# Kernel optimization log

Hardware: AMD Instinct MI355X
Metric: run time of the kernel (lower is better)

## Reference

```python
import jax, jax.numpy as jnp
import numpy as np

LMAX = 6
F_IN = 512      # sphere_fdim
F_HID = 8       # f_hidden
N_PTS = 192     # s2 healpix grid points (projector & feature-sphere kernel)
N_SO3GRID = 4000  # SO3Activation grid (resolution=10, ~20x10x20)
N_CONVGRID = 192  # so3_near_identity_grid (8 alpha x 3 beta x 8 gamma)
S2_DIM = (LMAX + 1) ** 2                            # 49
SO3_DIM = sum((2 * l + 1) ** 2 for l in range(LMAX + 1))  # 455
B = 128
C_ENC = 2048
H = W = 7


def setup_inputs() -> dict:
    key = jax.random.key(0)
    ks = jax.random.split(key, 11)
    return {
        "fmap": jax.random.normal(ks[0], (B, C_ENC, H, W), jnp.float32),
        "conv_w": jax.random.normal(ks[1], (F_IN, C_ENC), jnp.float32) / np.sqrt(C_ENC).astype(np.float32),
        "conv_b": jnp.zeros((F_IN,), jnp.float32),
        "proj_w": jax.random.uniform(ks[2], (H, W, N_PTS), jnp.float32) / (H * W),
        "proj_Y": jax.random.normal(ks[3], (N_PTS, S2_DIM), jnp.float32),
        "fs_w": jax.random.normal(ks[4], (F_IN, F_HID, N_PTS), jnp.float32),
        "fs_Y": jax.random.normal(ks[5], (N_PTS, S2_DIM), jnp.float32),
        "act_to": jax.random.normal(ks[6], (SO3_DIM, N_SO3GRID), jnp.float32) / np.sqrt(SO3_DIM).astype(np.float32),
        "act_from": jax.random.normal(ks[7], (N_SO3GRID, SO3_DIM), jnp.float32) / np.float32(N_SO3GRID),
        "so3_w": jax.random.normal(ks[8], (F_HID, 1, N_CONVGRID), jnp.float32),
        "so3_D": jax.random.normal(ks[9], (N_CONVGRID, SO3_DIM), jnp.float32),
    }


def _s2_to_so3_linear(x, psi, f_in):
    # e3nn o3.Linear(s2_irreps -> so3_irreps, internal_weights=False).
    # x: (B, f_in, S2_DIM) with per-l blocks of size 2l+1 (mul=1).
    # psi: (f_in, f_out, S2_DIM). Per l: outer product of input irrep with
    # weight irrep -> (2l+1)x(2l+1) Wigner block; path norm 1/sqrt(f_in*mul_in).
    outs = []
    for l in range(LMAX + 1):
        s, e = l * l, (l + 1) ** 2
        xl = x[:, :, s:e]          # (B, f_in, 2l+1)
        wl = psi[:, :, s:e]        # (f_in, f_out, 2l+1)
        ol = jnp.einsum('bfm,fgu->bgum', xl, wl) / np.sqrt(f_in).astype(np.float32)
        outs.append(ol.reshape(ol.shape[0], ol.shape[1], -1))
    return jnp.concatenate(outs, axis=-1)   # (B, f_out, SO3_DIM)


def _so3_to_so3_linear(x, psi, f_in):
    # e3nn o3.Linear(so3_irreps -> so3_irreps, internal_weights=False).
    # x: (B, f_in, SO3_DIM), per-l block (mul=2l+1, dim=2l+1) flattened [u, m].
    # psi: (f_in, f_out, SO3_DIM), per-l block (u_in, u_out).
    outs = []
    off = 0
    for l in range(LMAX + 1):
        d = 2 * l + 1
        xl = x[:, :, off:off + d * d].reshape(x.shape[0], f_in, d, d)
        wl = psi[:, :, off:off + d * d].reshape(f_in, psi.shape[1], d, d)
        ol = jnp.einsum('bfum,fguv->bgvm', xl, wl) / np.sqrt(f_in * d).astype(np.float32)
        outs.append(ol.reshape(ol.shape[0], ol.shape[1], -1))
        off += d * d
    return jnp.concatenate(outs, axis=-1)


def reference(fmap, conv_w, conv_b, proj_w, proj_Y, fs_w, fs_Y, act_to, act_from, so3_w, so3_D):
    # --- SpatialS2Projector: 1x1 conv, orthographic-grid weighting, S2 FT ---
    x = jnp.einsum('bchw,fc->bfhw', fmap, conv_w) + conv_b[None, :, None, None]
    x = jnp.einsum('bfhw,hwn->bfn', x, proj_w)                   # (B, 512, N_PTS)
    x = jnp.einsum('bfn,ni->bfi', x, proj_Y) / np.sqrt(N_PTS).astype(np.float32)  # (B, 512, 49)
    # --- feature sphere -> external weight for o3.Linear (S2 conv theorem) ---
    psi = jnp.einsum('fgn,ni->fgi', fs_w, fs_Y) / np.sqrt(N_PTS).astype(np.float32)  # (512, 8, 49)
    x = _s2_to_so3_linear(x, psi, F_IN)                          # (B, 8, 455)
    # --- SO3Activation: synthesize signal on SO3 grid, relu, analyze back ---
    g = jax.nn.relu(jnp.einsum('bfi,in->bfn', x, act_to))        # (B, 8, N_SO3GRID)
    x = jnp.einsum('bfn,ni->bfi', g, act_from)                   # (B, 8, 455)
    # --- SO3Convolution over near-identity grid ---
    psi2 = jnp.einsum('fgn,ni->fgi', so3_w, so3_D) / np.sqrt(N_CONVGRID).astype(np.float32)  # (8, 1, 455)
    x = _so3_to_so3_linear(x, psi2, F_HID)                       # (B, 1, 455)
    return x
```

## Files before the change

kernel.cpp:

```cpp
#include <hip/hip_runtime.h>
#include <hip/hip_bf16.h>

#define NB    128
#define CENC  2048
#define FIN   512
#define FHID  8
#define S2D   49
#define SO3D  455
#define HW    49

typedef unsigned short ushort_t;
typedef __bf16 bf16x8 __attribute__((ext_vector_type(8)));
typedef float  f32x4  __attribute__((ext_vector_type(4)));

__device__ __forceinline__ int soff(int l) { return l*(4*l*l-1)/3; }

__device__ __forceinline__ ushort_t f2bf(float x) {
  __hip_bfloat16 h = __float2bfloat16(x);
  return *reinterpret_cast<ushort_t*>(&h);
}
__device__ __forceinline__ float bf2f(ushort_t u) {
  __hip_bfloat16 h = *reinterpret_cast<__hip_bfloat16*>(&u);
  return __bfloat162float(h);
}


__device__ __forceinline__ void dev_gemm_nn(float* smem,
    const float* __restrict__ A, const float* __restrict__ B, float* __restrict__ C,
    int M, int N, int K, int lda, int ldb, int ldc, float alpha, int bx, int by)
{
  float* As = smem;
  float* Bs = smem + 32*68;
  const int tid = threadIdx.x;
  const int tx = tid & 15, ty = tid >> 4;
  const int n0 = bx * 64, m0 = by * 64;
  float acc[4][4] = {};
  for (int k0 = 0; k0 < K; k0 += 32) {
    {
      const int kk = tid & 31, mmB = tid >> 5;
      #pragma unroll
      for (int j = 0; j < 8; ++j) {
        const int mm = mmB + 8*j;
        const int m = m0 + mm, k = k0 + kk;
        As[kk*68 + mm] = (m < M && k < K) ? A[(size_t)m*lda + k] : 0.f;
      }
    }
    {
      const int nn = tid & 63, kkB = tid >> 6;
      #pragma unroll
      for (int j = 0; j < 8; ++j) {
        const int kk = kkB + 4*j;
        const int n = n0 + nn, k = k0 + kk;
        Bs[kk*68 + nn] = (n < N && k < K) ? B[(size_t)k*ldb + n] : 0.f;
      }
    }
    __syncthreads();
    #pragma unroll
    for (int kk = 0; kk < 32; ++kk) {
      const float4 a4 = *(const float4*)&As[kk*68 + ty*4];
      const float4 b4 = *(const float4*)&Bs[kk*68 + tx*4];
      const float av[4] = {a4.x,a4.y,a4.z,a4.w};
      const float bv[4] = {b4.x,b4.y,b4.z,b4.w};
      #pragma unroll
      for (int i = 0; i < 4; ++i)
        #pragma unroll
        for (int j = 0; j < 4; ++j)
          acc[i][j] = fmaf(av[i], bv[j], acc[i][j]);
    }
    __syncthreads();
  }
  #pragma unroll
  for (int i = 0; i < 4; ++i) {
    const int m = m0 + ty*4 + i;
    if (m >= M) continue;
    #pragma unroll
    for (int j = 0; j < 4; ++j) {
      const int n = n0 + tx*4 + j;
      if (n >= N) continue;
      C[(size_t)m*ldc + n] = acc[i][j] * alpha;
    }
  }
}

__device__ __forceinline__ void dev_transpose_cvt(float* smem,
    const float* __restrict__ in, int R, int C,
    ushort_t* __restrict__ out, int Rp, int Cp, int bx, int by)
{
  float (*t)[33] = (float(*)[33])smem;
  const int c0 = bx*32, r0 = by*32;
  const int tx = threadIdx.x & 31, ty = threadIdx.x >> 5;
  #pragma unroll
  for (int j = 0; j < 4; ++j) {
    const int r = r0 + ty + j*8, c = c0 + tx;
    t[ty + j*8][tx] = (r < R && c < C) ? in[(size_t)r*C + c] : 0.f;
  }
  __syncthreads();
  #pragma unroll
  for (int j = 0; j < 4; ++j) {
    const int c = c0 + ty + j*8, r = r0 + tx;
    if (c < Cp && r < Rp) out[(size_t)c*Rp + r] = f2bf(t[tx][ty + j*8]);
  }
}

__device__ __forceinline__ void dev_transpose_fmap(float* smem,
    const float* __restrict__ fmap, ushort_t* __restrict__ out, int cc, int b)
{
  float* Fs = smem;
  const int tid = threadIdx.x;
  const int c0 = cc*64;
  const float* fsrc = fmap + ((size_t)b*CENC + c0)*HW;
  for (int idx = tid; idx < 784; idx += 256)
    *(float4*)&Fs[idx*4] = *(const float4*)&fsrc[idx*4];
  __syncthreads();
  for (int idx = tid; idx < 3136; idx += 256) {
    const int h = idx >> 6, cl = idx & 63;
    out[(size_t)(b*49 + h)*CENC + c0 + cl] = f2bf(Fs[cl*49 + h]);
  }
}

__device__ __forceinline__ void dev_sumP(float* smem,
    const float* __restrict__ proj_w, const float* __restrict__ proj_Y,
    float* __restrict__ sumP)
{
  float* colsum = smem;
  const int tid = threadIdx.x;
  if (tid < 192) {
    float s = 0.f;
    for (int h = 0; h < 49; ++h) s += proj_w[h*192 + tid];
    colsum[tid] = s;
  }
  __syncthreads();
  if (tid < 64) {
    float s = 0.f;
    if (tid < 49) for (int k = 0; k < 192; ++k) s += colsum[k] * proj_Y[k*49 + tid];
    sumP[tid] = (tid < 49) ? s * 0.07216878364870323f : 0.f;
  }
}

__global__ __launch_bounds__(256) void prep_all(
    const float* __restrict__ fmap, const float* __restrict__ conv_w,
    const float* __restrict__ proj_w, const float* __restrict__ proj_Y,
    const float* __restrict__ fs_w, const float* __restrict__ fs_Y,
    const float* __restrict__ act_to, const float* __restrict__ act_from,
    const float* __restrict__ so3_w, const float* __restrict__ so3_D,
    float* __restrict__ wP, float* __restrict__ wSumP, float* __restrict__ wPsi2,
    float* __restrict__ wPsiP,
    ushort_t* __restrict__ actToT, ushort_t* __restrict__ actFromT,
    ushort_t* __restrict__ cwT, ushort_t* __restrict__ fmapT)
{
  __shared__ float smem[32*68*2];
  const int blk = blockIdx.x;
  const float is192 = 0.07216878364870323f;
  if (blk < 1) {
    dev_gemm_nn(smem, proj_w, proj_Y, wP, 49,49,192, 192,49,49, is192, 0, 0);
  } else if (blk < 9) {
    dev_gemm_nn(smem, so3_w, so3_D, wPsi2, 8,455,192, 192,455,455, is192, blk-1, 0);
  } else if (blk < 73) {
    dev_gemm_nn(smem, fs_w, fs_Y, wPsiP, 4096,49,192, 192,49,128, is192, 0, blk-9);
  } else if (blk < 2121) {
    const int t = blk-73;   dev_transpose_cvt(smem, act_to, 455, 4000, actToT, 512, 4096, t & 127, t >> 7);
  } else if (blk < 4169) {
    const int t = blk-2121; dev_transpose_cvt(smem, act_from, 4000, 455, actFromT, 4096, 512, t & 15, t >> 4);
  } else if (blk < 5193) {
    const int t = blk-4169; dev_transpose_cvt(smem, conv_w, 512, 2048, cwT, 512, 2048, t & 63, t >> 6);
  } else if (blk < 9289) {
    const int t = blk-5193; dev_transpose_fmap(smem, fmap, fmapT, t & 31, t >> 5);
  } else {
    dev_sumP(smem, proj_w, proj_Y, wSumP);
  }
}

__global__ __launch_bounds__(256) void psiT_bpsi(
    const float* __restrict__ wPsiP, const float* __restrict__ conv_b,
    ushort_t* __restrict__ psiT, float* __restrict__ bpsi, float* __restrict__ Tbuf)
{
  const int blk = blockIdx.x, tid = threadIdx.x;
  if (blk < 1024) {
    const int idx = blk*256 + tid;
    const int row = idx >> 9, f = idx & 511;
    const int g = row >> 6, ii = row & 63;
    psiT[idx] = (ii < 49) ? f2bf(wPsiP[(size_t)(f*8 + g)*128 + ii]) : (ushort_t)0;
  } else if (blk < 1152) {
    const int w = tid >> 6, lane = tid & 63;
    const int gi = (blk-1024)*4 + w;
    const int g = gi >> 6, ii = gi & 63;
    float s = 0.f;
    if (ii < 49) {
      #pragma unroll
      for (int s8 = 0; s8 < 8; ++s8) {
        const int f = s8*64 + lane;
        s += conv_b[f] * bf2f(f2bf(wPsiP[(size_t)(f*8 + g)*128 + ii]));
      }
    }
    #pragma unroll
    for (int off = 32; off; off >>= 1) s += __shfl_down(s, off);
    if (lane == 0) bpsi[gi] = s;
  } else {
    const int t = blk - 1152;
    float4* p = (float4*)Tbuf;
    const float4 z = (float4){0.f,0.f,0.f,0.f};
    #pragma unroll
    for (int j = 0; j < 4; ++j)
      p[t*1024 + j*256 + tid] = z;
  }
}

#define LSTR 72
__global__ __launch_bounds__(512) void gemm8_nt(
    const ushort_t* __restrict__ A, const ushort_t* __restrict__ B, void* __restrict__ Cv,
    int M, int N, int K, int lda, int ldb, int ldc,
    int mode, int kPartLen)
{
  __shared__ ushort_t Alds[128*LSTR];
  __shared__ ushort_t Blds[64*LSTR];
  const int tid  = threadIdx.x;
  const int wave = tid >> 6, lane = tid & 63;
  const int wm = wave >> 1, wn = wave & 1;
  const int col = lane & 15, quad = lane >> 4;
  const int m0 = blockIdx.y * 128, n0 = blockIdx.x * 64;
  int kStart = 0, kEnd = K;
  float*    C  = (float*)Cv;
  ushort_t* Cb = (ushort_t*)Cv;
  if (mode == 2) {
    kStart = blockIdx.z * kPartLen;
    kEnd = min(K, kStart + kPartLen);
    C += (size_t)blockIdx.z * (size_t)M * (size_t)ldc;
  } else if (mode == 4) {
    kStart = blockIdx.z * kPartLen;
    kEnd = min(K, kStart + kPartLen);
  }

  f32x4 acc[2][2];
  #pragma unroll
  for (int i = 0; i < 2; ++i)
    #pragma unroll
    for (int j = 0; j < 2; ++j)
      acc[i][j] = (f32x4){0.f,0.f,0.f,0.f};

  for (int k0 = kStart; k0 < kEnd; k0 += 64) {
    #pragma unroll
    for (int r = 0; r < 2; ++r) {
      const int u = tid + 512*r;
      const int mm = u >> 3, kg = u & 7;
      *(uint4*)&Alds[mm*LSTR + kg*8] = *(const uint4*)&A[(size_t)(m0+mm)*lda + k0 + kg*8];
    }
    {
      const int mm = tid >> 3, kg = tid & 7;
      if (mm < 64)
        *(uint4*)&Blds[mm*LSTR + kg*8] = *(const uint4*)&B[(size_t)(n0+mm)*ldb + k0 + kg*8];
    }
    __syncthreads();
    #pragma unroll
    for (int ks = 0; ks < 2; ++ks) {
      bf16x8 af[2], bfr[2];
      #pragma unroll
      for (int t = 0; t < 2; ++t) {
        af[t]  = *(bf16x8*)&Alds[(wm*32 + t*16 + col)*LSTR + ks*32 + quad*8];
        bfr[t] = *(bf16x8*)&Blds[(wn*32 + t*16 + col)*LSTR + ks*32 + quad*8];
      }
      #pragma unroll
      for (int i = 0; i < 2; ++i)
        #pragma unroll
        for (int j = 0; j < 2; ++j)
          acc[i][j] = __builtin_amdgcn_mfma_f32_16x16x32_bf16(af[i], bfr[j], acc[i][j], 0, 0, 0);
    }
    __syncthreads();
  }

  #pragma unroll
  for (int i = 0; i < 2; ++i) {
    const int mBase = m0 + wm*32 + i*16 + quad*4;
    #pragma unroll
    for (int j = 0; j < 2; ++j) {
      const int n = n0 + wn*32 + j*16 + col;
      if (mode == 1) {
        #pragma unroll
        for (int r = 0; r < 4; ++r)
          Cb[(size_t)(mBase+r)*ldc + n] = f2bf(fmaxf(acc[i][j][r], 0.f));
      } else if (mode == 3) {
        #pragma unroll
        for (int r = 0; r < 4; ++r)
          Cb[(size_t)(mBase+r)*ldc + n] = f2bf(acc[i][j][r]);
      } else if (mode == 4) {
        #pragma unroll
        for (int r = 0; r < 4; ++r)
          atomicAdd(&C[(size_t)(mBase+r)*ldc + n], acc[i][j][r]);
      } else {
        #pragma unroll
        for (int r = 0; r < 4; ++r)
          C[(size_t)(mBase+r)*ldc + n] = acc[i][j][r];
      }
    }
  }
}

__global__ __launch_bounds__(256) void gather_y(
    const float* __restrict__ T, const float* __restrict__ P,
    const float* __restrict__ sumP, const float* __restrict__ bpsi,
    ushort_t* __restrict__ y)
{
  __shared__ float Tg[49*64];
  __shared__ float Pl[49*49];
  __shared__ float sPl[49];
  __shared__ float bps[64];
  const int tid = threadIdx.x;
  const int g = blockIdx.x & 7, b = blockIdx.x >> 3;
  for (int idx = tid; idx < 49*64; idx += 256) {
    const int h = idx >> 6, c = idx & 63;
    Tg[idx] = T[(size_t)(b*49 + h)*512 + g*64 + c];
  }
  for (int idx = tid; idx < 2401; idx += 256) Pl[idx] = P[idx];
  if (tid < 49) sPl[tid] = sumP[tid];
  if (tid < 64) bps[tid] = bpsi[g*64 + tid];
  __syncthreads();
  #pragma unroll
  for (int rr = 0; rr < 2; ++rr) {
    const int j = tid + rr*256;
    float v = 0.f;
    if (j < SO3D) {
      int l;
      if (j < 1) l = 0; else if (j < 10) l = 1; else if (j < 35) l = 2;
      else if (j < 84) l = 3; else if (j < 165) l = 4; else if (j < 286) l = 5; else l = 6;
      const int so = soff(l), d = 2*l+1;
      const int r = j - so;
      const int u = r / d, m = r - u*d;
      const int i = l*l + m, colT = l*l + u;
      float acc = 0.f;
      #pragma unroll 7
      for (int h = 0; h < 49; ++h)
        acc = fmaf(Pl[h*49 + i], Tg[h*64 + colT], acc);
      v = (acc + sPl[i]*bps[colT]) * 0.044194173824159216f;
    }
    y[(size_t)(b*8+g)*512 + j] = f2bf(v);
  }
}

__global__ __launch_bounds__(512) void so3_final(
    const float* __restrict__ zpart, const float* __restrict__ psi2,
    float* __restrict__ out)
{
  __shared__ float Zs[8*SO3D];
  __shared__ float P2s[8*SO3D];
  const int b = blockIdx.x, tid = threadIdx.x;
  for (int idx = tid; idx < 8*SO3D; idx += 512) {
    const int f = idx / SO3D, i = idx - f*SO3D;
    float s = 0.f;
    #pragma unroll
    for (int p = 0; p < 8; ++p)
      s += zpart[((size_t)p*1024 + (size_t)b*FHID + f)*512 + i];
    Zs[idx] = s;
    P2s[idx] = psi2[idx];
  }
  __syncthreads();
  if (tid < SO3D) {
    const int i = tid;
    int l;
    if (i < 1) l = 0; else if (i < 10) l = 1; else if (i < 35) l = 2;
    else if (i < 84) l = 3; else if (i < 165) l = 4; else if (i < 286) l = 5; else l = 6;
    const int so = soff(l), d = 2*l+1;
    const int r = i - so;
    const int v = r / d, m = r - v*d;
    float acc = 0.f;
    for (int f = 0; f < 8; ++f)
      for (int u = 0; u < d; ++u)
        acc = fmaf(Zs[f*SO3D + so + u*d + m], P2s[f*SO3D + so + u*d + v], acc);
    const float scale = rsqrtf(8.0f * (float)d);
    out[(size_t)b*SO3D + i] = acc * scale;
  }
}

extern "C" void kernel_launch(void* const* d_in, const int* in_sizes, int n_in,
                              void* d_out, int out_size, void* d_ws, size_t ws_size,
                              hipStream_t stream) {
  const float* fmap    = (const float*)d_in[0];
  const float* conv_w  = (const float*)d_in[1];
  const float* conv_b  = (const float*)d_in[2];
  const float* proj_w  = (const float*)d_in[3];
  const float* proj_Y  = (const float*)d_in[4];
  const float* fs_w    = (const float*)d_in[5];
  const float* fs_Y    = (const float*)d_in[6];
  const float* act_to  = (const float*)d_in[7];
  const float* act_from= (const float*)d_in[8];
  const float* so3_w   = (const float*)d_in[9];
  const float* so3_D   = (const float*)d_in[10];
  float* out           = (float*)d_out;

  char* wsb = (char*)d_ws;
  float*    wP       = (float*)(wsb + 0);
  float*    wSumP    = (float*)(wsb + 9728);
  float*    wPsi2    = (float*)(wsb + 9984);
  ushort_t* actToT   = (ushort_t*)(wsb + 24576);
  ushort_t* actFromT = (ushort_t*)(wsb + 4218880);
  ushort_t* yPad     = (ushort_t*)(wsb + 8413184);
  ushort_t* psiT     = (ushort_t*)(wsb + 9461760);
  float*    bpsi     = (float*)(wsb + 9986048);
  ushort_t* W2T      = (ushort_t*)(wsb + 9988096);
  ushort_t* fmapT    = (ushort_t*)(wsb + 12085248);
  float*    wPsiP    = (float*)(wsb + 37775360);
  ushort_t* cwT      = (ushort_t*)(wsb + 39872512);
  float*    Tbuf     = (float*)(wsb + 41969664);
  ushort_t* gBuf     = (ushort_t*)(wsb + 12085248);
  float*    zPart    = (float*)(wsb + 20473856);

  prep_all<<<dim3(9290), 256, 0, stream>>>(
      fmap, conv_w, proj_w, proj_Y, fs_w, fs_Y, act_to, act_from, so3_w, so3_D,
      wP, wSumP, wPsi2, wPsiP, actToT, actFromT, cwT, fmapT);
  psiT_bpsi<<<dim3(1936), 256, 0, stream>>>(wPsiP, conv_b, psiT, bpsi, Tbuf);
  gemm8_nt<<<dim3(32,4), 512, 0, stream>>>(psiT, cwT, W2T,
      512, 2048, 512, 512, 512, 2048, 3, 0);
  gemm8_nt<<<dim3(8,49,2), 512, 0, stream>>>(fmapT, W2T, Tbuf,
      6272, 512, 2048, 2048, 2048, 512, 4, 1024);
  gather_y<<<dim3(1024), 256, 0, stream>>>(Tbuf, wP, wSumP, bpsi, yPad);
  gemm8_nt<<<dim3(64,8), 512, 0, stream>>>(yPad, actToT, gBuf,
      1024, 4096, 512, 512, 512, 4096, 1, 0);
  gemm8_nt<<<dim3(8,8,8), 512, 0, stream>>>(gBuf, actFromT, zPart,
      1024, 512, 4096, 4096, 4096, 512, 2, 512);
  so3_final<<<dim3(128), 512, 0, stream>>>(zPart, wPsi2, out);
}
```

Measured before the change: 254.4 us.

## Rewrite bf16 GEMM with direct global-to-LDS loads, XOR swizzle, 64x128 tiles

Replaces the 512-thread 128x64-tile GEMM with a 256-thread 64x128-tile kernel. Tiles are loaded straight into LDS through global_load_lds, and an XOR swizzle replaces padding to avoid bank conflicts. The split-K atomic accumulation for the fmap GEMM is dropped in favour of a full-K pass with direct stores, which also removes the Tbuf zeroing blocks. This cuts register staging and atomic traffic, but the fmap GEMM now runs with fewer blocks and there is still no double buffering.

```diff
diff --git a/kernel.cpp b/kernel.cpp
--- a/kernel.cpp
+++ b/kernel.cpp
@@ -12,6 +12,10 @@
 typedef unsigned short ushort_t;
 typedef __bf16 bf16x8 __attribute__((ext_vector_type(8)));
 typedef float  f32x4  __attribute__((ext_vector_type(4)));
+
+#define GLD16(gp, lp) __builtin_amdgcn_global_load_lds( \
+    (__attribute__((address_space(1))) const unsigned int*)(gp), \
+    (__attribute__((address_space(3))) unsigned int*)(lp), 16, 0, 0)
 
 __device__ __forceinline__ int soff(int l) { return l*(4*l*l-1)/3; }
 
@@ -172,7 +176,7 @@
 
 __global__ __launch_bounds__(256) void psiT_bpsi(
     const float* __restrict__ wPsiP, const float* __restrict__ conv_b,
-    ushort_t* __restrict__ psiT, float* __restrict__ bpsi, float* __restrict__ Tbuf)
+    ushort_t* __restrict__ psiT, float* __restrict__ bpsi)
 {
   const int blk = blockIdx.x, tid = threadIdx.x;
   if (blk < 1024) {
@@ -180,7 +184,7 @@
     const int row = idx >> 9, f = idx & 511;
     const int g = row >> 6, ii = row & 63;
     psiT[idx] = (ii < 49) ? f2bf(wPsiP[(size_t)(f*8 + g)*128 + ii]) : (ushort_t)0;
-  } else if (blk < 1152) {
+  } else {
     const int w = tid >> 6, lane = tid & 63;
     const int gi = (blk-1024)*4 + w;
     const int g = gi >> 6, ii = gi & 63;
@@ -195,29 +199,20 @@
     #pragma unroll
     for (int off = 32; off; off >>= 1) s += __shfl_down(s, off);
     if (lane == 0) bpsi[gi] = s;
-  } else {
-    const int t = blk - 1152;
-    float4* p = (float4*)Tbuf;
-    const float4 z = (float4){0.f,0.f,0.f,0.f};
-    #pragma unroll
-    for (int j = 0; j < 4; ++j)
-      p[t*1024 + j*256 + tid] = z;
-  }
-}
-
-#define LSTR 72
-__global__ __launch_bounds__(512) void gemm8_nt(
+  }
+}
+
+__global__ __launch_bounds__(256) void gemm4_nt(
     const ushort_t* __restrict__ A, const ushort_t* __restrict__ B, void* __restrict__ Cv,
     int M, int N, int K, int lda, int ldb, int ldc,
     int mode, int kPartLen)
 {
-  __shared__ ushort_t Alds[128*LSTR];
-  __shared__ ushort_t Blds[64*LSTR];
-  const int tid  = threadIdx.x;
-  const int wave = tid >> 6, lane = tid & 63;
-  const int wm = wave >> 1, wn = wave & 1;
-  const int col = lane & 15, quad = lane >> 4;
-  const int m0 = blockIdx.y * 128, n0 = blockIdx.x * 64;
+  __shared__ ushort_t Alds[64*64];
+  __shared__ ushort_t Blds[128*64];
+  const int tid = threadIdx.x;
+  const int wv = tid >> 6, ln = tid & 63;
+  const int col = ln & 15, quad = ln >> 4;
+  const int m0 = blockIdx.y * 64, n0 = blockIdx.x * 128;
   int kStart = 0, kEnd = K;
   float*    C  = (float*)Cv;
   ushort_t* Cb = (ushort_t*)Cv;
@@ -225,41 +220,53 @@
     kStart = blockIdx.z * kPartLen;
     kEnd = min(K, kStart + kPartLen);
     C += (size_t)blockIdx.z * (size_t)M * (size_t)ldc;
-  } else if (mode == 4) {
-    kStart = blockIdx.z * kPartLen;
-    kEnd = min(K, kStart + kPartLen);
-  }
-
-  f32x4 acc[2][2];
-  #pragma unroll
-  for (int i = 0; i < 2; ++i)
+  }
+
+  const int rl = ln >> 3;
+  const int gsw = (ln & 7) ^ rl;
+  const ushort_t* aP[2]; const ushort_t* bP[4];
+  ushort_t* aL[2]; ushort_t* bL[4];
+  #pragma unroll
+  for (int r = 0; r < 2; ++r) {
+    const int R = wv*16 + r*8;
+    aP[r] = A + (size_t)(m0 + R + rl)*lda + kStart + gsw*8;
+    aL[r] = &Alds[R*64];
+  }
+  #pragma unroll
+  for (int r = 0; r < 4; ++r) {
+    const int R = wv*32 + r*8;
+    bP[r] = B + (size_t)(n0 + R + rl)*ldb + kStart + gsw*8;
+    bL[r] = &Blds[R*64];
+  }
+
+  f32x4 acc[4][2];
+  #pragma unroll
+  for (int i = 0; i < 4; ++i)
     #pragma unroll
     for (int j = 0; j < 2; ++j)
       acc[i][j] = (f32x4){0.f,0.f,0.f,0.f};
 
   for (int k0 = kStart; k0 < kEnd; k0 += 64) {
     #pragma unroll
-    for (int r = 0; r < 2; ++r) {
-      const int u = tid + 512*r;
-      const int mm = u >> 3, kg = u & 7;
-      *(uint4*)&Alds[mm*LSTR + kg*8] = *(const uint4*)&A[(size_t)(m0+mm)*lda + k0 + kg*8];
-    }
-    {
-      const int mm = tid >> 3, kg = tid & 7;
-      if (mm < 64)
-        *(uint4*)&Blds[mm*LSTR + kg*8] = *(const uint4*)&B[(size_t)(n0+mm)*ldb + k0 + kg*8];
-    }
+    for (int r = 0; r < 2; ++r) { GLD16(aP[r], aL[r]); aP[r] += 64; }
+    #pragma unroll
+    for (int r = 0; r < 4; ++r) { GLD16(bP[r], bL[r]); bP[r] += 64; }
     __syncthreads();
     #pragma unroll
     for (int ks = 0; ks < 2; ++ks) {
-      bf16x8 af[2], bfr[2];
-      #pragma unroll
-      for (int t = 0; t < 2; ++t) {
-        af[t]  = *(bf16x8*)&Alds[(wm*32 + t*16 + col)*LSTR + ks*32 + quad*8];
-        bfr[t] = *(bf16x8*)&Blds[(wn*32 + t*16 + col)*LSTR + ks*32 + quad*8];
-      }
-      #pragma unroll
-      for (int i = 0; i < 2; ++i)
+      bf16x8 af[4], bfr[2];
+      #pragma unroll
+      for (int i = 0; i < 4; ++i) {
+        const int row = i*16 + col;
+        af[i] = *(bf16x8*)&Alds[row*64 + (((ks*4 + quad) ^ (row & 7)) << 3)];
+      }
+      #pragma unroll
+      for (int j = 0; j < 2; ++j) {
+        const int row = wv*32 + j*16 + col;
+        bfr[j] = *(bf16x8*)&Blds[row*64 + (((ks*4 + quad) ^ (row & 7)) << 3)];
+      }
+      #pragma unroll
+      for (int i = 0; i < 4; ++i)
         #pragma unroll
         for (int j = 0; j < 2; ++j)
           acc[i][j] = __builtin_amdgcn_mfma_f32_16x16x32_bf16(af[i], bfr[j], acc[i][j], 0, 0, 0);
@@ -268,11 +275,11 @@
   }
 
   #pragma unroll
-  for (int i = 0; i < 2; ++i) {
-    const int mBase = m0 + wm*32 + i*16 + quad*4;
+  for (int i = 0; i < 4; ++i) {
+    const int mBase = m0 + i*16 + quad*4;
     #pragma unroll
     for (int j = 0; j < 2; ++j) {
-      const int n = n0 + wn*32 + j*16 + col;
+      const int n = n0 + wv*32 + j*16 + col;
       if (mode == 1) {
         #pragma unroll
         for (int r = 0; r < 4; ++r)
@@ -281,10 +288,6 @@
         #pragma unroll
         for (int r = 0; r < 4; ++r)
           Cb[(size_t)(mBase+r)*ldc + n] = f2bf(acc[i][j][r]);
-      } else if (mode == 4) {
-        #pragma unroll
-        for (int r = 0; r < 4; ++r)
-          atomicAdd(&C[(size_t)(mBase+r)*ldc + n], acc[i][j][r]);
       } else {
         #pragma unroll
         for (int r = 0; r < 4; ++r)
@@ -405,15 +408,15 @@
   prep_all<<<dim3(9290), 256, 0, stream>>>(
       fmap, conv_w, proj_w, proj_Y, fs_w, fs_Y, act_to, act_from, so3_w, so3_D,
       wP, wSumP, wPsi2, wPsiP, actToT, actFromT, cwT, fmapT);
-  psiT_bpsi<<<dim3(1936), 256, 0, stream>>>(wPsiP, conv_b, psiT, bpsi, Tbuf);
-  gemm8_nt<<<dim3(32,4), 512, 0, stream>>>(psiT, cwT, W2T,
+  psiT_bpsi<<<dim3(1152), 256, 0, stream>>>(wPsiP, conv_b, psiT, bpsi);
+  gemm4_nt<<<dim3(16,8), 256, 0, stream>>>(psiT, cwT, W2T,
       512, 2048, 512, 512, 512, 2048, 3, 0);
-  gemm8_nt<<<dim3(8,49,2), 512, 0, stream>>>(fmapT, W2T, Tbuf,
-      6272, 512, 2048, 2048, 2048, 512, 4, 1024);
+  gemm4_nt<<<dim3(4,98), 256, 0, stream>>>(fmapT, W2T, Tbuf,
+      6272, 512, 2048, 2048, 2048, 512, 0, 0);
   gather_y<<<dim3(1024), 256, 0, stream>>>(Tbuf, wP, wSumP, bpsi, yPad);
-  gemm8_nt<<<dim3(64,8), 512, 0, stream>>>(yPad, actToT, gBuf,
+  gemm4_nt<<<dim3(32,16), 256, 0, stream>>>(yPad, actToT, gBuf,
       1024, 4096, 512, 512, 512, 4096, 1, 0);
-  gemm8_nt<<<dim3(8,8,8), 512, 0, stream>>>(gBuf, actFromT, zPart,
+  gemm4_nt<<<dim3(4,16,8), 256, 0, stream>>>(gBuf, actFromT, zPart,
       1024, 512, 4096, 4096, 4096, 512, 2, 512);
   so3_final<<<dim3(128), 512, 0, stream>>>(zPart, wPsi2, out);
 }
```

After: 230.7 us. 9.3% less time.
